# Kernel optimization log

Measured on AMD Instinct MI355X. Metric: run time of the kernel, lower is better.

Reference implementation:

```python
import jax, jax.numpy as jnp
import numpy as np

BETA = 0.25  # commitment/codebook mixing as in VQVAE.__init__


def setup_inputs() -> dict:
    key = jax.random.key(0)
    k1, k2 = jax.random.split(key)
    # z: encoder latent [B, C, H, W] with C = latent_dim
    z = jax.random.normal(k1, (32, 64, 64, 64), dtype=jnp.float32)
    # codebook: nn.Embedding(num_embeddings, latent_dim).weight
    codebook = jax.random.normal(k2, (1024, 64), dtype=jnp.float32)
    return {"z": z, "codebook": codebook}


def reference(z, codebook):
    B, C, H, W = z.shape
    zf = z.reshape(B, C, H * W).transpose(0, 2, 1)  # [B, N, C], N = H*W
    # Squared Euclidean distances; argmin identical to torch.cdist(p=2) argmin
    # since sqrt is monotone (min_distances are unused in the original forward).
    d2 = (jnp.sum(zf * zf, axis=-1, keepdims=True)              # [B, N, 1]
          + jnp.sum(codebook * codebook, axis=-1)[None, None, :]  # [1, 1, K]
          - 2.0 * jnp.einsum('bnc,kc->bnk', zf, codebook))        # [B, N, K]
    indices = jnp.argmin(d2, axis=-1)                            # [B, N]
    z_q = codebook[indices]                                      # [B, N, C] gather
    z_q = z_q.transpose(0, 2, 1).reshape(B, C, H, W)
    commitment_loss = jnp.mean((jax.lax.stop_gradient(z_q) - z) ** 2)
    codebook_loss = jnp.mean((z_q - jax.lax.stop_gradient(z)) ** 2)
    loss = commitment_loss + BETA * codebook_loss
    return z_q, loss
```

## Files before the change

### kernel.cpp

```cpp
#include <hip/hip_runtime.h>
#include <float.h>

#define HW    4096
#define NC    64
#define NK    1024
#define NB    32
#define NPIX  (NB*HW)
#define TOTAL (NPIX*NC)
#define PPB   128

#define MARGIN 8e-3f

typedef __attribute__((ext_vector_type(8))) short short8;
typedef __attribute__((ext_vector_type(4))) float floatx4;

__device__ __forceinline__ unsigned short f2bf(float f) {
    unsigned u = __float_as_uint(f);
    u += 0x7FFFu + ((u >> 16) & 1u);
    return (unsigned short)(u >> 16);
}
__device__ __forceinline__ float bf2f(unsigned short h) {
    return __uint_as_float(((unsigned)h) << 16);
}

__global__ void vq_prep_kernel(const float* __restrict__ cb,
                               float* __restrict__ cnorm,
                               unsigned short* __restrict__ cb_hi,
                               unsigned short* __restrict__ cb_lo,
                               float* __restrict__ loss_out) {
    const int b = blockIdx.x;
    if (b < 64) {
        const int i = b * 256 + threadIdx.x;
        if (i == 0) loss_out[0] = 0.0f;
        float4 v = ((const float4*)cb)[i];
        unsigned short h0 = f2bf(v.x), h1 = f2bf(v.y),
                       h2 = f2bf(v.z), h3 = f2bf(v.w);
        unsigned short l0 = f2bf(v.x - bf2f(h0)), l1 = f2bf(v.y - bf2f(h1)),
                       l2 = f2bf(v.z - bf2f(h2)), l3 = f2bf(v.w - bf2f(h3));
        uint2 ph = make_uint2((unsigned)h0 | ((unsigned)h1 << 16),
                              (unsigned)h2 | ((unsigned)h3 << 16));
        uint2 pl = make_uint2((unsigned)l0 | ((unsigned)l1 << 16),
                              (unsigned)l2 | ((unsigned)l3 << 16));
        ((uint2*)cb_hi)[i] = ph;
        ((uint2*)cb_lo)[i] = pl;
    } else {
        const int k = (b - 64) * 256 + threadIdx.x;
        const float4* r4 = (const float4*)(cb + (size_t)k * NC);
        double s = 0.0;
        #pragma unroll
        for (int j = 0; j < 16; ++j) {
            float4 v = r4[j];
            s = fma((double)v.x, (double)v.x, s);
            s = fma((double)v.y, (double)v.y, s);
            s = fma((double)v.z, (double)v.z, s);
            s = fma((double)v.w, (double)v.w, s);
        }
        cnorm[k] = (float)s;
    }
}

__global__ __launch_bounds__(256, 4) void vq_mfma_kernel(
        const float* __restrict__ z,
        const float* __restrict__ cb,
        const unsigned short* __restrict__ cb_hi,
        const unsigned short* __restrict__ cb_lo,
        const float* __restrict__ cnorm,
        float* __restrict__ zq,
        float* __restrict__ loss_out) {
    __shared__ alignas(16) uint4 abuf[512];
    __shared__ alignas(16) float cn_lds[NK];
    __shared__ int   finidx[PPB];
    __shared__ int   flags[PPB];
    __shared__ float redf[4];

    const int tid = threadIdx.x;
    const int g0  = blockIdx.x * PPB;
    const int bb  = g0 >> 12;
    const int pp0 = g0 & 4095;
    const float* zbase = z  + (size_t)bb * (NC * HW) + pp0;
    float*      zqbase = zq + (size_t)bb * (NC * HW) + pp0;

    ((float4*)cn_lds)[tid] = ((const float4*)cnorm)[tid];

    const int lane = tid & 63;
    const int w    = tid >> 6;
    const int q    = lane >> 4;
    const int pcol = lane & 15;

    float zraw[2][2][8];
    #pragma unroll
    for (int ks = 0; ks < 2; ++ks)
        #pragma unroll
        for (int j = 0; j < 2; ++j)
            #pragma unroll
            for (int t = 0; t < 8; ++t)
                zraw[ks][j][t] = zbase[(size_t)(ks * 32 + q * 8 + t) * HW
                                       + (w * 32 + j * 16 + pcol)];
    short8 Bh[2][2], Bl[2][2];
    #pragma unroll
    for (int ks = 0; ks < 2; ++ks)
        #pragma unroll
        for (int j = 0; j < 2; ++j)
            #pragma unroll
            for (int t = 0; t < 8; ++t) {
                float v = -2.0f * zraw[ks][j][t];
                unsigned short h = f2bf(v);
                unsigned short l = f2bf(v - bf2f(h));
                Bh[ks][j][t] = (short)h;
                Bl[ks][j][t] = (short)l;
            }

    const int spart = tid >> 7;
    const int sidx  = tid & 127;
    const int srow  = sidx >> 3;
    const int schk  = sidx & 7;
    const int ldst  = spart * 128 + srow * 8 + (schk ^ (srow & 7));
    const char* gsrc = (spart == 0 ? (const char*)cb_hi : (const char*)cb_lo)
                       + (size_t)sidx * 16;

    const int ridx0 = pcol * 8 + (q ^ (pcol & 7));
    const int ridx1 = pcol * 8 + ((4 + q) ^ (pcol & 7));

    uint4 sreg = *(const uint4*)(gsrc);
    abuf[ldst] = sreg;
    sreg = *(const uint4*)(gsrc + 2048);
    __syncthreads();

    float B1[2] = {FLT_MAX, FLT_MAX};
    float B2[2] = {FLT_MAX, FLT_MAX};
    int   I1[2] = {0, 0};

    #pragma unroll 2
    for (int tile = 0; tile < 64; ++tile) {
        if (tile < 63) abuf[((tile + 1) & 1) * 256 + ldst] = sreg;
        if (tile < 62) sreg = *(const uint4*)(gsrc + (size_t)(tile + 2) * 2048);

        const short8* A = (const short8*)abuf + (tile & 1) * 256;
        short8 ah0 = A[ridx0];
        short8 ah1 = A[ridx1];
        short8 al0 = A[128 + ridx0];
        short8 al1 = A[128 + ridx1];

        const floatx4 cn4 = *(const floatx4*)&cn_lds[tile * 16 + q * 4];
        const int kb = tile * 16 + q * 4;
        #pragma unroll
        for (int j = 0; j < 2; ++j) {
            floatx4 a0 = __builtin_amdgcn_mfma_f32_16x16x32_bf16(ah0, Bh[0][j], cn4, 0, 0, 0);
            floatx4 a1 = {0.f, 0.f, 0.f, 0.f};
            a1 = __builtin_amdgcn_mfma_f32_16x16x32_bf16(ah1, Bh[1][j], a1, 0, 0, 0);
            a0 = __builtin_amdgcn_mfma_f32_16x16x32_bf16(ah0, Bl[0][j], a0, 0, 0, 0);
            a1 = __builtin_amdgcn_mfma_f32_16x16x32_bf16(ah1, Bl[1][j], a1, 0, 0, 0);
            a0 = __builtin_amdgcn_mfma_f32_16x16x32_bf16(al0, Bh[0][j], a0, 0, 0, 0);
            a1 = __builtin_amdgcn_mfma_f32_16x16x32_bf16(al1, Bh[1][j], a1, 0, 0, 0);

            #pragma unroll
            for (int i = 0; i < 4; ++i) {
                float s = a0[i] + a1[i];
                bool lt = s < B1[j];
                I1[j] = lt ? (kb + i) : I1[j];
                B2[j] = __builtin_amdgcn_fmed3f(s, B1[j], B2[j]);
                B1[j] = fminf(s, B1[j]);
            }
        }
        __syncthreads();
    }

    #pragma unroll
    for (int j = 0; j < 2; ++j) {
        float b1 = B1[j], b2 = B2[j];
        int i1 = I1[j];
        #pragma unroll
        for (int d = 16; d <= 32; d <<= 1) {
            float ob1 = __shfl_xor(b1, d);
            float ob2 = __shfl_xor(b2, d);
            int   oi1 = __shfl_xor(i1, d);
            float nb2 = fminf(fmaxf(b1, ob1), fminf(b2, ob2));
            bool lt = (ob1 < b1) || (ob1 == b1 && oi1 < i1);
            b1 = lt ? ob1 : b1;
            i1 = lt ? oi1 : i1;
            b2 = nb2;
        }
        if (q == 0) {
            const int px = w * 32 + j * 16 + pcol;
            finidx[px] = i1;
            flags[px]  = (b2 - b1 < MARGIN) ? 1 : 0;
        }
    }
    int myflag = 0;
    __syncthreads();
    if (tid < PPB) myflag = flags[tid];
    const int nflag = __syncthreads_count(myflag);

    if (nflag > 0) {
        double* red_s = reinterpret_cast<double*>(cn_lds);
        int*    red_i = reinterpret_cast<int*>(cn_lds + 512);
        for (int p = 0; p < PPB; ++p) {
            if (flags[p]) {
                const float* zp = zbase + p;
                double bd = 1.0e300; int bi = 0;
                #pragma unroll 1
                for (int r = 0; r < 4; ++r) {
                    const int k = tid * 4 + r;
                    const float* rowp = cb + (size_t)k * NC;
                    double s = 0.0;
                    for (int c = 0; c < NC; ++c) {
                        double t = (double)zp[(size_t)c * HW] - (double)rowp[c];
                        s = fma(t, t, s);
                    }
                    if (s < bd) { bd = s; bi = k; }
                }
                red_s[tid] = bd; red_i[tid] = bi;
                __syncthreads();
                if (tid < 64) {
                    double m = red_s[tid]; int mi = red_i[tid];
                    #pragma unroll
                    for (int t = 1; t < 4; ++t) {
                        double om = red_s[tid + 64 * t];
                        int    oi = red_i[tid + 64 * t];
                        if (om < m || (om == m && oi < mi)) { m = om; mi = oi; }
                    }
                    #pragma unroll
                    for (int off = 32; off > 0; off >>= 1) {
                        double om = __shfl_down(m, off);
                        int    oi = __shfl_down(mi, off);
                        if (om < m || (om == m && oi < mi)) { m = om; mi = oi; }
                    }
                    if (tid == 0) finidx[p] = mi;
                }
                __syncthreads();
            }
        }
        __syncthreads();
    }

    {
        const int p  = tid & (PPB - 1);
        const int qq = tid >> 7;
        const int fi = finidx[p];
        const float4* crow4 = (const float4*)(cb + (size_t)fi * NC) + qq * 8;
        float sse = 0.f;
        #pragma unroll
        for (int j = 0; j < 8; ++j) {
            const float4 qv = crow4[j];
            const size_t c0 = (size_t)(qq * 32 + 4 * j) * HW + p;
            const float z0 = zbase[c0];
            const float z1 = zbase[c0 + HW];
            const float z2 = zbase[c0 + 2 * (size_t)HW];
            const float z3 = zbase[c0 + 3 * (size_t)HW];
            zqbase[c0]                  = qv.x;
            zqbase[c0 + HW]             = qv.y;
            zqbase[c0 + 2 * (size_t)HW] = qv.z;
            zqbase[c0 + 3 * (size_t)HW] = qv.w;
            float t0 = qv.x - z0, t1 = qv.y - z1, t2 = qv.z - z2, t3 = qv.w - z3;
            sse = fmaf(t0, t0, sse);
            sse = fmaf(t1, t1, sse);
            sse = fmaf(t2, t2, sse);
            sse = fmaf(t3, t3, sse);
        }
        #pragma unroll
        for (int off = 32; off > 0; off >>= 1) sse += __shfl_down(sse, off);
        if ((tid & 63) == 0) redf[tid >> 6] = sse;
        __syncthreads();
        if (tid == 0)
            atomicAdd(loss_out, (redf[0] + redf[1] + redf[2] + redf[3]) *
                                (1.25f / (float)TOTAL));
    }
}

extern "C" void kernel_launch(void* const* d_in, const int* in_sizes, int n_in,
                              void* d_out, int out_size, void* d_ws, size_t ws_size,
                              hipStream_t stream) {
    const float* z  = (const float*)d_in[0];
    const float* cb = (const float*)d_in[1];
    float* out      = (float*)d_out;
    float* zqp      = out;
    float* loss     = out + TOTAL;

    float* cnorm          = (float*)d_ws;
    unsigned short* cb_hi = (unsigned short*)((char*)d_ws + 4096);
    unsigned short* cb_lo = (unsigned short*)((char*)d_ws + 4096 + NK * NC * 2);

    vq_prep_kernel<<<68, 256, 0, stream>>>(cb, cnorm, cb_hi, cb_lo, loss);
    vq_mfma_kernel<<<NPIX / PPB, 256, 0, stream>>>(z, cb, cb_hi, cb_lo, cnorm,
                                                   zqp, loss);
}
```

Before: 178.1 us.

## Load codebook MFMA operands directly from global memory, drop LDS staging

Removes the double-buffered LDS staging of the bf16 hi/lo codebook tiles and the per-tile __syncthreads. Each lane now loads its MFMA A operands straight from global memory (mostly L2-resident), with a two-tile register prefetch. This targets the block-wide barrier stalls and LDS traffic in the main loop. In exchange, every wave issues redundant global loads of the same codebook data, which adds cache bandwidth pressure and VGPR use.

```diff
diff --git a/kernel.cpp b/kernel.cpp
--- a/kernel.cpp
+++ b/kernel.cpp
@@ -67,7 +67,6 @@
         const float* __restrict__ cnorm,
         float* __restrict__ zq,
         float* __restrict__ loss_out) {
-    __shared__ alignas(16) uint4 abuf[512];
     __shared__ alignas(16) float cn_lds[NK];
     __shared__ int   finidx[PPB];
     __shared__ int   flags[PPB];
@@ -110,37 +109,17 @@
                 Bl[ks][j][t] = (short)l;
             }
 
-    const int spart = tid >> 7;
-    const int sidx  = tid & 127;
-    const int srow  = sidx >> 3;
-    const int schk  = sidx & 7;
-    const int ldst  = spart * 128 + srow * 8 + (schk ^ (srow & 7));
-    const char* gsrc = (spart == 0 ? (const char*)cb_hi : (const char*)cb_lo)
-                       + (size_t)sidx * 16;
-
-    const int ridx0 = pcol * 8 + (q ^ (pcol & 7));
-    const int ridx1 = pcol * 8 + ((4 + q) ^ (pcol & 7));
-
-    uint4 sreg = *(const uint4*)(gsrc);
-    abuf[ldst] = sreg;
-    sreg = *(const uint4*)(gsrc + 2048);
+    const char* pAh = (const char*)cb_hi + pcol * 128 + q * 16;
+    const char* pAl = (const char*)cb_lo + pcol * 128 + q * 16;
+
     __syncthreads();
 
     float B1[2] = {FLT_MAX, FLT_MAX};
     float B2[2] = {FLT_MAX, FLT_MAX};
     int   I1[2] = {0, 0};
 
-    #pragma unroll 2
-    for (int tile = 0; tile < 64; ++tile) {
-        if (tile < 63) abuf[((tile + 1) & 1) * 256 + ldst] = sreg;
-        if (tile < 62) sreg = *(const uint4*)(gsrc + (size_t)(tile + 2) * 2048);
-
-        const short8* A = (const short8*)abuf + (tile & 1) * 256;
-        short8 ah0 = A[ridx0];
-        short8 ah1 = A[ridx1];
-        short8 al0 = A[128 + ridx0];
-        short8 al1 = A[128 + ridx1];
-
+    auto tile_body = [&](short8 ah0, short8 ah1, short8 al0, short8 al1,
+                         int tile) {
         const floatx4 cn4 = *(const floatx4*)&cn_lds[tile * 16 + q * 4];
         const int kb = tile * 16 + q * 4;
         #pragma unroll
@@ -162,8 +141,24 @@
                 B1[j] = fminf(s, B1[j]);
             }
         }
-        __syncthreads();
-    }
+    };
+
+    #define LDA(H0, H1, L0, L1, T)                                          \
+        H0 = *(const short8*)(pAh + (size_t)(T) * 2048);                    \
+        H1 = *(const short8*)(pAh + (size_t)(T) * 2048 + 64);               \
+        L0 = *(const short8*)(pAl + (size_t)(T) * 2048);                    \
+        L1 = *(const short8*)(pAl + (size_t)(T) * 2048 + 64);
+
+    short8 pH0, pH1, pL0, pL1, qH0, qH1, qL0, qL1;
+    LDA(pH0, pH1, pL0, pL1, 0)
+    LDA(qH0, qH1, qL0, qL1, 1)
+    for (int t = 0; t < 64; t += 2) {
+        tile_body(pH0, pH1, pL0, pL1, t);
+        if (t < 62) { LDA(pH0, pH1, pL0, pL1, t + 2) }
+        tile_body(qH0, qH1, qL0, qL1, t + 1);
+        if (t < 62) { LDA(qH0, qH1, qL0, qL1, t + 3) }
+    }
+    #undef LDA
 
     #pragma unroll
     for (int j = 0; j < 2; ++j) {
```

Result: slower. 244.6 us (+37.3%).

## Stage codebook tiles with direct global-to-LDS loads, four tiles per barrier

Applied to the files above, without the earlier changes.

Codebook hi/lo bf16 tiles are now copied with global_load_lds straight into shared memory instead of going through a register and then a shared-memory store. The XOR swizzle moves from the LDS destination to the global source address. Each double-buffered stage now covers four 16-entry tiles, so the main loop runs 16 iterations with one barrier each instead of 64. This cuts VGPR staging, store instructions and barrier count, at the cost of quadrupling the LDS used for codebook tiles, which may limit occupancy. It also relies on the compiler placing the right vmcnt waits before the async data is read.

```diff
diff --git a/kernel.cpp b/kernel.cpp
--- a/kernel.cpp
+++ b/kernel.cpp
@@ -67,8 +67,8 @@
         const float* __restrict__ cnorm,
         float* __restrict__ zq,
         float* __restrict__ loss_out) {
-    __shared__ alignas(16) uint4 abuf[512];
-    __shared__ alignas(16) float cn_lds[NK];
+    __shared__ alignas(16) uint4  abuf[2][1024];
+    __shared__ alignas(16) float  cn_lds[NK];
     __shared__ int   finidx[PPB];
     __shared__ int   flags[PPB];
     __shared__ float redf[4];
@@ -86,6 +86,25 @@
     const int w    = tid >> 6;
     const int q    = lane >> 4;
     const int pcol = lane & 15;
+
+    const int  sidx  = tid & 127;
+    const int  spart = tid >> 7;
+    const int  sswz  = (sidx & ~7) | ((sidx & 7) ^ ((sidx >> 3) & 7));
+    const char* gsrc = (spart == 0 ? (const char*)cb_hi : (const char*)cb_lo)
+                       + (size_t)sswz * 16;
+
+    auto stage_iv = [&](int iv, int buf) {
+        #pragma unroll
+        for (int tt = 0; tt < 4; ++tt)
+            __builtin_amdgcn_global_load_lds(
+                (const __attribute__((address_space(1))) void*)
+                    (gsrc + (size_t)iv * 8192 + (size_t)tt * 2048),
+                (__attribute__((address_space(3))) void*)
+                    &abuf[buf][tt * 256 + tid],
+                16, 0, 0);
+    };
+
+    stage_iv(0, 0);
 
     float zraw[2][2][8];
     #pragma unroll
@@ -110,37 +129,17 @@
                 Bl[ks][j][t] = (short)l;
             }
 
-    const int spart = tid >> 7;
-    const int sidx  = tid & 127;
-    const int srow  = sidx >> 3;
-    const int schk  = sidx & 7;
-    const int ldst  = spart * 128 + srow * 8 + (schk ^ (srow & 7));
-    const char* gsrc = (spart == 0 ? (const char*)cb_hi : (const char*)cb_lo)
-                       + (size_t)sidx * 16;
-
     const int ridx0 = pcol * 8 + (q ^ (pcol & 7));
     const int ridx1 = pcol * 8 + ((4 + q) ^ (pcol & 7));
 
-    uint4 sreg = *(const uint4*)(gsrc);
-    abuf[ldst] = sreg;
-    sreg = *(const uint4*)(gsrc + 2048);
     __syncthreads();
 
     float B1[2] = {FLT_MAX, FLT_MAX};
     float B2[2] = {FLT_MAX, FLT_MAX};
     int   I1[2] = {0, 0};
 
-    #pragma unroll 2
-    for (int tile = 0; tile < 64; ++tile) {
-        if (tile < 63) abuf[((tile + 1) & 1) * 256 + ldst] = sreg;
-        if (tile < 62) sreg = *(const uint4*)(gsrc + (size_t)(tile + 2) * 2048);
-
-        const short8* A = (const short8*)abuf + (tile & 1) * 256;
-        short8 ah0 = A[ridx0];
-        short8 ah1 = A[ridx1];
-        short8 al0 = A[128 + ridx0];
-        short8 al1 = A[128 + ridx1];
-
+    auto tile_body = [&](short8 ah0, short8 ah1, short8 al0, short8 al1,
+                         int tile) {
         const floatx4 cn4 = *(const floatx4*)&cn_lds[tile * 16 + q * 4];
         const int kb = tile * 16 + q * 4;
         #pragma unroll
@@ -161,6 +160,20 @@
                 B2[j] = __builtin_amdgcn_fmed3f(s, B1[j], B2[j]);
                 B1[j] = fminf(s, B1[j]);
             }
+        }
+    };
+
+    for (int iv = 0; iv < 16; ++iv) {
+        if (iv < 15) stage_iv(iv + 1, (iv + 1) & 1);
+        const short8* Abase = (const short8*)&abuf[iv & 1][0];
+        #pragma unroll
+        for (int tt = 0; tt < 4; ++tt) {
+            const short8* A = Abase + tt * 256;
+            short8 ah0 = A[ridx0];
+            short8 ah1 = A[ridx1];
+            short8 al0 = A[128 + ridx0];
+            short8 al1 = A[128 + ridx1];
+            tile_body(ah0, ah1, al0, al1, iv * 4 + tt);
         }
         __syncthreads();
     }
```

Measured after the change: 173.6 us. 1.03x faster.
